# Performance work log

Measured on AMD Instinct MI355X. Metric: run time of the kernel, lower is better.

The kernel has to match this reference:

```python
import jax, jax.numpy as jnp
import numpy as np

N, D = 66560, 128      # total actor rows, embedding dim
M = 16384              # anchor count (scenes x vehicles)
P, NEG = 3, 63         # positives per anchor, negatives per anchor
EPS = 1e-8             # torch nn.CosineSimilarity eps


def setup_inputs() -> dict:
    key = jax.random.key(0)
    k1, k2, k3, k4, k5 = jax.random.split(key, 5)
    return {
        "ids_fut": jax.random.normal(k1, (N, D), dtype=jnp.float32),
        "ids_hist": jax.random.normal(k2, (N, D), dtype=jnp.float32),
        "anchor_idx": jax.random.randint(k3, (M,), 0, N),
        "pos_idx": jax.random.randint(k4, (M, P), 0, N),
        "neg_idx": jax.random.randint(k5, (M, NEG), 0, N),
    }


def _cos_plus_one(anchor, samples):
    # anchor: [M, D], samples: [M, K, D] -> cosine sim + 1, per torch CosineSimilarity
    dot = jnp.einsum("md,mkd->mk", anchor, samples)
    na = jnp.linalg.norm(anchor, axis=-1)[:, None]          # [M, 1]
    ns = jnp.linalg.norm(samples, axis=-1)                  # [M, K]
    return dot / jnp.maximum(na * ns, EPS) + 1.0


def reference(ids_fut, ids_hist, anchor_idx, pos_idx, neg_idx):
    anchor = ids_hist[anchor_idx]          # [M, D]
    pos = ids_fut[pos_idx]                 # [M, P, D]
    neg = ids_fut[neg_idx]                 # [M, NEG, D]
    sp = jnp.sum(_cos_plus_one(anchor, pos), axis=1)   # [M]
    sn = jnp.sum(_cos_plus_one(anchor, neg), axis=1)   # [M]
    sim_loss = -jnp.log(sp / (sp + sn))                 # [M]
    loss_tot = jnp.sum(sim_loss)           # 'repres_loss'; 'repres_loss_cnt' == M (constant)
    return loss_tot
```

## Files before the change

### kernel.cpp

```cpp
#include <hip/hip_runtime.h>
#include <math.h>

#define DIM 128
#define P_POS 3
#define N_NEG 63
#define SCALE 16.0f

typedef float floatx2 __attribute__((ext_vector_type(2)));

#if defined(__has_builtin)
#if __has_builtin(__builtin_elementwise_fma)
#define HAVE_EFMA 1
#endif
#endif

__device__ __forceinline__ floatx2 pkfma(floatx2 a, floatx2 b, floatx2 c) {
#ifdef HAVE_EFMA
    return __builtin_elementwise_fma(a, b, c);
#else
    floatx2 r;
    r.x = fmaf(a.x, b.x, c.x);
    r.y = fmaf(a.y, b.y, c.y);
    return r;
#endif
}

__device__ __forceinline__ float wave_reduce_sum(float v) {
#pragma unroll
    for (int off = 32; off > 0; off >>= 1) v += __shfl_xor(v, off, 64);
    return v;
}
__device__ __forceinline__ float g8_reduce(float v) {
#pragma unroll
    for (int off = 4; off > 0; off >>= 1) v += __shfl_xor(v, off, 64);
    return v;
}
__device__ __forceinline__ float g32_reduce(float v) {
#pragma unroll
    for (int off = 16; off > 0; off >>= 1) v += __shfl_xor(v, off, 64);
    return v;
}

__global__ __launch_bounds__(256) void prep_fp8_kernel(const float* __restrict__ fut,
                                                       unsigned* __restrict__ futq,
                                                       int nrows) {
    int half = threadIdx.x >> 5;
    int l = threadIdx.x & 31;
    int row = blockIdx.x * 8 + half;
    if (row >= nrows) return;
    float4 x = *reinterpret_cast<const float4*>(fut + (size_t)row * DIM + l * 4);
    float ss = x.x * x.x;
    ss = fmaf(x.y, x.y, ss);
    ss = fmaf(x.z, x.z, ss);
    ss = fmaf(x.w, x.w, ss);
    ss = g32_reduce(ss);
    float r = (ss > 0.f) ? rsqrtf(ss) * SCALE : 0.f;
    int w = __builtin_amdgcn_cvt_pk_fp8_f32(x.x * r, x.y * r, 0, false);
    w = __builtin_amdgcn_cvt_pk_fp8_f32(x.z * r, x.w * r, w, true);
    futq[(size_t)row * 32 + l] = (unsigned)w;
}

__global__ __launch_bounds__(256) void idloss_fp8w_kernel(
    const float* __restrict__ hist, const int* __restrict__ anchor_idx,
    const int* __restrict__ pos_idx, const int* __restrict__ neg_idx,
    const uint4* __restrict__ futq, float* __restrict__ partials) {
    __shared__ float smem[4];
    const int wave = threadIdx.x >> 6;
    const int lane = threadIdx.x & 63;
    const int m = __builtin_amdgcn_readfirstlane(blockIdx.x * 4 + wave);
    const int g = lane >> 3;
    const int t = lane & 7;

    int nidx = (lane < N_NEG) ? neg_idx[m * N_NEG + lane] : 0;

    const int aidx = anchor_idx[m];
    const int p0 = pos_idx[m * P_POS + 0];
    const int p1 = pos_idx[m * P_POS + 1];
    const int p2 = pos_idx[m * P_POS + 2];
    int pidx = (g == 1) ? p1 : (g == 2) ? p2 : p0;

    const float4* ap =
        reinterpret_cast<const float4*>(hist + (size_t)aidx * DIM + t * 16);
    float4 A0 = ap[0], A1 = ap[1], A2 = ap[2], A3 = ap[3];
    float ss = A0.x * A0.x;
    ss = fmaf(A0.y, A0.y, ss); ss = fmaf(A0.z, A0.z, ss); ss = fmaf(A0.w, A0.w, ss);
    ss = fmaf(A1.x, A1.x, ss); ss = fmaf(A1.y, A1.y, ss);
    ss = fmaf(A1.z, A1.z, ss); ss = fmaf(A1.w, A1.w, ss);
    ss = fmaf(A2.x, A2.x, ss); ss = fmaf(A2.y, A2.y, ss);
    ss = fmaf(A2.z, A2.z, ss); ss = fmaf(A2.w, A2.w, ss);
    ss = fmaf(A3.x, A3.x, ss); ss = fmaf(A3.y, A3.y, ss);
    ss = fmaf(A3.z, A3.z, ss); ss = fmaf(A3.w, A3.w, ss);
    ss = g8_reduce(ss);
    float rna = (ss > 0.f) ? rsqrtf(ss) * (1.0f / SCALE) : 0.f;
    floatx2 av0, av1, av2, av3, av4, av5, av6, av7;
    av0.x = A0.x * rna; av0.y = A0.y * rna;
    av1.x = A0.z * rna; av1.y = A0.w * rna;
    av2.x = A1.x * rna; av2.y = A1.y * rna;
    av3.x = A1.z * rna; av3.y = A1.w * rna;
    av4.x = A2.x * rna; av4.y = A2.y * rna;
    av5.x = A2.z * rna; av5.y = A2.w * rna;
    av6.x = A3.x * rna; av6.y = A3.y * rna;
    av7.x = A3.z * rna; av7.y = A3.w * rna;

    int js[8];
#pragma unroll
    for (int k = 0; k < 8; ++k) js[k] = __shfl(nidx, 8 * k + g, 64);

    uint4 vp = futq[(size_t)pidx * 8 + t];
    if (g >= P_POS) { vp.x = vp.y = vp.z = vp.w = 0u; }
    uint4 vs[8];
#pragma unroll
    for (int k = 0; k < 8; ++k) {
        vs[k] = futq[(size_t)js[k] * 8 + t];
        if (8 * k + g >= N_NEG) { vs[k].x = vs[k].y = vs[k].z = vs[k].w = 0u; }
    }

    floatx2 n0 = {0.f, 0.f}, n1 = {0.f, 0.f}, n2 = {0.f, 0.f}, n3 = {0.f, 0.f};
#pragma unroll
    for (int k = 0; k < 8; ++k) {
        uint4 v = vs[k];
        n0 = pkfma(__builtin_amdgcn_cvt_pk_f32_fp8(v.x, false), av0, n0);
        n1 = pkfma(__builtin_amdgcn_cvt_pk_f32_fp8(v.x, true), av1, n1);
        n2 = pkfma(__builtin_amdgcn_cvt_pk_f32_fp8(v.y, false), av2, n2);
        n3 = pkfma(__builtin_amdgcn_cvt_pk_f32_fp8(v.y, true), av3, n3);
        n0 = pkfma(__builtin_amdgcn_cvt_pk_f32_fp8(v.z, false), av4, n0);
        n1 = pkfma(__builtin_amdgcn_cvt_pk_f32_fp8(v.z, true), av5, n1);
        n2 = pkfma(__builtin_amdgcn_cvt_pk_f32_fp8(v.w, false), av6, n2);
        n3 = pkfma(__builtin_amdgcn_cvt_pk_f32_fp8(v.w, true), av7, n3);
    }
    floatx2 pa = {0.f, 0.f}, pb = {0.f, 0.f};
    pa = pkfma(__builtin_amdgcn_cvt_pk_f32_fp8(vp.x, false), av0, pa);
    pb = pkfma(__builtin_amdgcn_cvt_pk_f32_fp8(vp.x, true), av1, pb);
    pa = pkfma(__builtin_amdgcn_cvt_pk_f32_fp8(vp.y, false), av2, pa);
    pb = pkfma(__builtin_amdgcn_cvt_pk_f32_fp8(vp.y, true), av3, pb);
    pa = pkfma(__builtin_amdgcn_cvt_pk_f32_fp8(vp.z, false), av4, pa);
    pb = pkfma(__builtin_amdgcn_cvt_pk_f32_fp8(vp.z, true), av5, pb);
    pa = pkfma(__builtin_amdgcn_cvt_pk_f32_fp8(vp.w, false), av6, pa);
    pb = pkfma(__builtin_amdgcn_cvt_pk_f32_fp8(vp.w, true), av7, pb);

    floatx2 ns = (n0 + n1) + (n2 + n3);
    floatx2 ps = pa + pb;
    float accn = wave_reduce_sum(ns.x + ns.y);
    float accp = wave_reduce_sum(ps.x + ps.y);

    if (lane == 0) {
        float sp = accp + (float)P_POS;
        float sn = accn + (float)N_NEG;
        smem[wave] = -logf(sp / (sp + sn));
    }
    __syncthreads();
    if (threadIdx.x == 0)
        partials[blockIdx.x] = smem[0] + smem[1] + smem[2] + smem[3];
}

__global__ __launch_bounds__(1024) void reduce1024_kernel(
    const float* __restrict__ partials, float* __restrict__ out, int n4) {
    __shared__ float smem[16];
    const int tid = threadIdx.x;
    const int lane = tid & 63;
    const int wid = tid >> 6;
    float acc = 0.f;
    for (int i = tid; i < n4; i += 1024) {
        float4 v = reinterpret_cast<const float4*>(partials)[i];
        acc += (v.x + v.y) + (v.z + v.w);
    }
    acc = wave_reduce_sum(acc);
    if (lane == 0) smem[wid] = acc;
    __syncthreads();
    if (tid == 0) {
        float s = 0.f;
#pragma unroll
        for (int i = 0; i < 16; ++i) s += smem[i];
        out[0] = s;
    }
}

extern "C" void kernel_launch(void* const* d_in, const int* in_sizes, int n_in,
                              void* d_out, int out_size, void* d_ws, size_t ws_size,
                              hipStream_t stream) {
    const float* fut  = (const float*)d_in[0];
    const float* hist = (const float*)d_in[1];
    const int* anchor_idx = (const int*)d_in[2];
    const int* pos_idx    = (const int*)d_in[3];
    const int* neg_idx    = (const int*)d_in[4];

    int N = in_sizes[0] / DIM;
    int M = in_sizes[2];
    int main_blocks = M / 4;

    size_t futq_bytes = (size_t)N * 32 * sizeof(unsigned);
    unsigned* futq = (unsigned*)d_ws;
    float* partials = (float*)((char*)d_ws + futq_bytes);

    int prep_blocks = (N + 7) / 8;
    prep_fp8_kernel<<<prep_blocks, 256, 0, stream>>>(fut, futq, N);
    idloss_fp8w_kernel<<<main_blocks, 256, 0, stream>>>(hist, anchor_idx, pos_idx,
                                                        neg_idx, (const uint4*)futq,
                                                        partials);
    reduce1024_kernel<<<1, 1024, 0, stream>>>(partials, (float*)d_out,
                                              main_blocks / 4);
}
```

Baseline: 31.12 us.

## Process two anchors per wavefront and write per-anchor partials directly

Measured after the change: 33.42 us. 7.4% more time.

```diff
diff --git a/kernel.cpp b/kernel.cpp
--- a/kernel.cpp
+++ b/kernel.cpp
@@ -29,6 +29,15 @@
 #pragma unroll
     for (int off = 32; off > 0; off >>= 1) v += __shfl_xor(v, off, 64);
     return v;
+}
+__device__ __forceinline__ void wave_reduce4(float& a, float& b, float& c, float& d) {
+#pragma unroll
+    for (int off = 32; off > 0; off >>= 1) {
+        a += __shfl_xor(a, off, 64);
+        b += __shfl_xor(b, off, 64);
+        c += __shfl_xor(c, off, 64);
+        d += __shfl_xor(d, off, 64);
+    }
 }
 __device__ __forceinline__ float g8_reduce(float v) {
 #pragma unroll
@@ -60,97 +69,129 @@
     futq[(size_t)row * 32 + l] = (unsigned)w;
 }
 
-__global__ __launch_bounds__(256) void idloss_fp8w_kernel(
+__device__ __forceinline__ void dq8(uint4 v, const floatx2* av, floatx2& x, floatx2& y,
+                                    floatx2& z, floatx2& w) {
+    x = pkfma(__builtin_amdgcn_cvt_pk_f32_fp8(v.x, false), av[0], x);
+    y = pkfma(__builtin_amdgcn_cvt_pk_f32_fp8(v.x, true), av[1], y);
+    z = pkfma(__builtin_amdgcn_cvt_pk_f32_fp8(v.y, false), av[2], z);
+    w = pkfma(__builtin_amdgcn_cvt_pk_f32_fp8(v.y, true), av[3], w);
+    x = pkfma(__builtin_amdgcn_cvt_pk_f32_fp8(v.z, false), av[4], x);
+    y = pkfma(__builtin_amdgcn_cvt_pk_f32_fp8(v.z, true), av[5], y);
+    z = pkfma(__builtin_amdgcn_cvt_pk_f32_fp8(v.w, false), av[6], z);
+    w = pkfma(__builtin_amdgcn_cvt_pk_f32_fp8(v.w, true), av[7], w);
+}
+
+__global__ __launch_bounds__(256) void idloss_fp8d_kernel(
     const float* __restrict__ hist, const int* __restrict__ anchor_idx,
     const int* __restrict__ pos_idx, const int* __restrict__ neg_idx,
     const uint4* __restrict__ futq, float* __restrict__ partials) {
-    __shared__ float smem[4];
     const int wave = threadIdx.x >> 6;
     const int lane = threadIdx.x & 63;
-    const int m = __builtin_amdgcn_readfirstlane(blockIdx.x * 4 + wave);
+    const int m0 = __builtin_amdgcn_readfirstlane((blockIdx.x * 4 + wave) * 2);
+    const int m1 = m0 + 1;
     const int g = lane >> 3;
     const int t = lane & 7;
 
-    int nidx = (lane < N_NEG) ? neg_idx[m * N_NEG + lane] : 0;
-
-    const int aidx = anchor_idx[m];
-    const int p0 = pos_idx[m * P_POS + 0];
-    const int p1 = pos_idx[m * P_POS + 1];
-    const int p2 = pos_idx[m * P_POS + 2];
-    int pidx = (g == 1) ? p1 : (g == 2) ? p2 : p0;
-
-    const float4* ap =
-        reinterpret_cast<const float4*>(hist + (size_t)aidx * DIM + t * 16);
-    float4 A0 = ap[0], A1 = ap[1], A2 = ap[2], A3 = ap[3];
-    float ss = A0.x * A0.x;
-    ss = fmaf(A0.y, A0.y, ss); ss = fmaf(A0.z, A0.z, ss); ss = fmaf(A0.w, A0.w, ss);
-    ss = fmaf(A1.x, A1.x, ss); ss = fmaf(A1.y, A1.y, ss);
-    ss = fmaf(A1.z, A1.z, ss); ss = fmaf(A1.w, A1.w, ss);
-    ss = fmaf(A2.x, A2.x, ss); ss = fmaf(A2.y, A2.y, ss);
-    ss = fmaf(A2.z, A2.z, ss); ss = fmaf(A2.w, A2.w, ss);
-    ss = fmaf(A3.x, A3.x, ss); ss = fmaf(A3.y, A3.y, ss);
-    ss = fmaf(A3.z, A3.z, ss); ss = fmaf(A3.w, A3.w, ss);
-    ss = g8_reduce(ss);
-    float rna = (ss > 0.f) ? rsqrtf(ss) * (1.0f / SCALE) : 0.f;
-    floatx2 av0, av1, av2, av3, av4, av5, av6, av7;
-    av0.x = A0.x * rna; av0.y = A0.y * rna;
-    av1.x = A0.z * rna; av1.y = A0.w * rna;
-    av2.x = A1.x * rna; av2.y = A1.y * rna;
-    av3.x = A1.z * rna; av3.y = A1.w * rna;
-    av4.x = A2.x * rna; av4.y = A2.y * rna;
-    av5.x = A2.z * rna; av5.y = A2.w * rna;
-    av6.x = A3.x * rna; av6.y = A3.y * rna;
-    av7.x = A3.z * rna; av7.y = A3.w * rna;
-
-    int js[8];
-#pragma unroll
-    for (int k = 0; k < 8; ++k) js[k] = __shfl(nidx, 8 * k + g, 64);
-
-    uint4 vp = futq[(size_t)pidx * 8 + t];
-    if (g >= P_POS) { vp.x = vp.y = vp.z = vp.w = 0u; }
-    uint4 vs[8];
+    int nidx0 = (lane < N_NEG) ? neg_idx[m0 * N_NEG + lane] : 0;
+    int nidx1 = (lane < N_NEG) ? neg_idx[m1 * N_NEG + lane] : 0;
+    const int aidx0 = anchor_idx[m0];
+    const int aidx1 = anchor_idx[m1];
+    const int p00 = pos_idx[m0 * P_POS + 0];
+    const int p01 = pos_idx[m0 * P_POS + 1];
+    const int p02 = pos_idx[m0 * P_POS + 2];
+    const int p10 = pos_idx[m1 * P_POS + 0];
+    const int p11 = pos_idx[m1 * P_POS + 1];
+    const int p12 = pos_idx[m1 * P_POS + 2];
+    int pidx0 = (g == 1) ? p01 : (g == 2) ? p02 : p00;
+    int pidx1 = (g == 1) ? p11 : (g == 2) ? p12 : p10;
+
+    const float4* apA =
+        reinterpret_cast<const float4*>(hist + (size_t)aidx0 * DIM + t * 16);
+    const float4* apB =
+        reinterpret_cast<const float4*>(hist + (size_t)aidx1 * DIM + t * 16);
+    float4 A[4], B[4];
+#pragma unroll
+    for (int i = 0; i < 4; ++i) A[i] = apA[i];
+#pragma unroll
+    for (int i = 0; i < 4; ++i) B[i] = apB[i];
+
+    float ssA = 0.f, ssB = 0.f;
+#pragma unroll
+    for (int i = 0; i < 4; ++i) {
+        ssA = fmaf(A[i].x, A[i].x, ssA); ssA = fmaf(A[i].y, A[i].y, ssA);
+        ssA = fmaf(A[i].z, A[i].z, ssA); ssA = fmaf(A[i].w, A[i].w, ssA);
+        ssB = fmaf(B[i].x, B[i].x, ssB); ssB = fmaf(B[i].y, B[i].y, ssB);
+        ssB = fmaf(B[i].z, B[i].z, ssB); ssB = fmaf(B[i].w, B[i].w, ssB);
+    }
+    ssA = g8_reduce(ssA);
+    ssB = g8_reduce(ssB);
+    float rnaA = (ssA > 0.f) ? rsqrtf(ssA) * (1.0f / SCALE) : 0.f;
+    float rnaB = (ssB > 0.f) ? rsqrtf(ssB) * (1.0f / SCALE) : 0.f;
+    floatx2 avA[8], avB[8];
+#pragma unroll
+    for (int i = 0; i < 4; ++i) {
+        avA[2 * i].x = A[i].x * rnaA; avA[2 * i].y = A[i].y * rnaA;
+        avA[2 * i + 1].x = A[i].z * rnaA; avA[2 * i + 1].y = A[i].w * rnaA;
+        avB[2 * i].x = B[i].x * rnaB; avB[2 * i].y = B[i].y * rnaB;
+        avB[2 * i + 1].x = B[i].z * rnaB; avB[2 * i + 1].y = B[i].w * rnaB;
+    }
+
+    int jsA[8], jsB[8];
+#pragma unroll
+    for (int k = 0; k < 8; ++k) jsA[k] = __shfl(nidx0, 8 * k + g, 64);
+#pragma unroll
+    for (int k = 0; k < 8; ++k) jsB[k] = __shfl(nidx1, 8 * k + g, 64);
+
+    uint4 vpA = futq[(size_t)pidx0 * 8 + t];
+    uint4 vpB = futq[(size_t)pidx1 * 8 + t];
+    if (g >= P_POS) {
+        vpA.x = vpA.y = vpA.z = vpA.w = 0u;
+        vpB.x = vpB.y = vpB.z = vpB.w = 0u;
+    }
+    uint4 vsA[8], vsB[8];
 #pragma unroll
     for (int k = 0; k < 8; ++k) {
-        vs[k] = futq[(size_t)js[k] * 8 + t];
-        if (8 * k + g >= N_NEG) { vs[k].x = vs[k].y = vs[k].z = vs[k].w = 0u; }
-    }
-
-    floatx2 n0 = {0.f, 0.f}, n1 = {0.f, 0.f}, n2 = {0.f, 0.f}, n3 = {0.f, 0.f};
+        vsA[k] = futq[(size_t)jsA[k] * 8 + t];
+        if (8 * k + g >= N_NEG) { vsA[k].x = vsA[k].y = vsA[k].z = vsA[k].w = 0u; }
+    }
 #pragma unroll
     for (int k = 0; k < 8; ++k) {
-        uint4 v = vs[k];
-        n0 = pkfma(__builtin_amdgcn_cvt_pk_f32_fp8(v.x, false), av0, n0);
-        n1 = pkfma(__builtin_amdgcn_cvt_pk_f32_fp8(v.x, true), av1, n1);
-        n2 = pkfma(__builtin_amdgcn_cvt_pk_f32_fp8(v.y, false), av2, n2);
-        n3 = pkfma(__builtin_amdgcn_cvt_pk_f32_fp8(v.y, true), av3, n3);
-        n0 = pkfma(__builtin_amdgcn_cvt_pk_f32_fp8(v.z, false), av4, n0);
-        n1 = pkfma(__builtin_amdgcn_cvt_pk_f32_fp8(v.z, true), av5, n1);
-        n2 = pkfma(__builtin_amdgcn_cvt_pk_f32_fp8(v.w, false), av6, n2);
-        n3 = pkfma(__builtin_amdgcn_cvt_pk_f32_fp8(v.w, true), av7, n3);
-    }
-    floatx2 pa = {0.f, 0.f}, pb = {0.f, 0.f};
-    pa = pkfma(__builtin_amdgcn_cvt_pk_f32_fp8(vp.x, false), av0, pa);
-    pb = pkfma(__builtin_amdgcn_cvt_pk_f32_fp8(vp.x, true), av1, pb);
-    pa = pkfma(__builtin_amdgcn_cvt_pk_f32_fp8(vp.y, false), av2, pa);
-    pb = pkfma(__builtin_amdgcn_cvt_pk_f32_fp8(vp.y, true), av3, pb);
-    pa = pkfma(__builtin_amdgcn_cvt_pk_f32_fp8(vp.z, false), av4, pa);
-    pb = pkfma(__builtin_amdgcn_cvt_pk_f32_fp8(vp.z, true), av5, pb);
-    pa = pkfma(__builtin_amdgcn_cvt_pk_f32_fp8(vp.w, false), av6, pa);
-    pb = pkfma(__builtin_amdgcn_cvt_pk_f32_fp8(vp.w, true), av7, pb);
-
-    floatx2 ns = (n0 + n1) + (n2 + n3);
-    floatx2 ps = pa + pb;
-    float accn = wave_reduce_sum(ns.x + ns.y);
-    float accp = wave_reduce_sum(ps.x + ps.y);
+        vsB[k] = futq[(size_t)jsB[k] * 8 + t];
+        if (8 * k + g >= N_NEG) { vsB[k].x = vsB[k].y = vsB[k].z = vsB[k].w = 0u; }
+    }
+
+    floatx2 nA0 = {0.f, 0.f}, nA1 = {0.f, 0.f}, nA2 = {0.f, 0.f}, nA3 = {0.f, 0.f};
+#pragma unroll
+    for (int k = 0; k < 8; ++k) dq8(vsA[k], avA, nA0, nA1, nA2, nA3);
+    floatx2 pA0 = {0.f, 0.f}, pA1 = {0.f, 0.f}, pA2 = {0.f, 0.f}, pA3 = {0.f, 0.f};
+    dq8(vpA, avA, pA0, pA1, pA2, pA3);
+
+    floatx2 nB0 = {0.f, 0.f}, nB1 = {0.f, 0.f}, nB2 = {0.f, 0.f}, nB3 = {0.f, 0.f};
+#pragma unroll
+    for (int k = 0; k < 8; ++k) dq8(vsB[k], avB, nB0, nB1, nB2, nB3);
+    floatx2 pB0 = {0.f, 0.f}, pB1 = {0.f, 0.f}, pB2 = {0.f, 0.f}, pB3 = {0.f, 0.f};
+    dq8(vpB, avB, pB0, pB1, pB2, pB3);
+
+    floatx2 nsA = (nA0 + nA1) + (nA2 + nA3);
+    floatx2 psA = (pA0 + pA1) + (pA2 + pA3);
+    floatx2 nsB = (nB0 + nB1) + (nB2 + nB3);
+    floatx2 psB = (pB0 + pB1) + (pB2 + pB3);
+    float accnA = nsA.x + nsA.y;
+    float accpA = psA.x + psA.y;
+    float accnB = nsB.x + nsB.y;
+    float accpB = psB.x + psB.y;
+    wave_reduce4(accnA, accpA, accnB, accpB);
 
     if (lane == 0) {
-        float sp = accp + (float)P_POS;
-        float sn = accn + (float)N_NEG;
-        smem[wave] = -logf(sp / (sp + sn));
-    }
-    __syncthreads();
-    if (threadIdx.x == 0)
-        partials[blockIdx.x] = smem[0] + smem[1] + smem[2] + smem[3];
+        float spA = accpA + (float)P_POS;
+        float snA = accnA + (float)N_NEG;
+        float spB = accpB + (float)P_POS;
+        float snB = accnB + (float)N_NEG;
+        float2 r;
+        r.x = -logf(spA / (spA + snA));
+        r.y = -logf(spB / (spB + snB));
+        *reinterpret_cast<float2*>(partials + m0) = r;
+    }
 }
 
 __global__ __launch_bounds__(1024) void reduce1024_kernel(
@@ -186,7 +227,7 @@
 
     int N = in_sizes[0] / DIM;
     int M = in_sizes[2];
-    int main_blocks = M / 4;
+    int main_blocks = M / 8;
 
     size_t futq_bytes = (size_t)N * 32 * sizeof(unsigned);
     unsigned* futq = (unsigned*)d_ws;
@@ -194,9 +235,8 @@
 
     int prep_blocks = (N + 7) / 8;
     prep_fp8_kernel<<<prep_blocks, 256, 0, stream>>>(fut, futq, N);
-    idloss_fp8w_kernel<<<main_blocks, 256, 0, stream>>>(hist, anchor_idx, pos_idx,
+    idloss_fp8d_kernel<<<main_blocks, 256, 0, stream>>>(hist, anchor_idx, pos_idx,
                                                         neg_idx, (const uint4*)futq,
                                                         partials);
-    reduce1024_kernel<<<1, 1024, 0, stream>>>(partials, (float*)d_out,
-                                              main_blocks / 4);
-}
+    reduce1024_kernel<<<1, 1024, 0, stream>>>(partials, (float*)d_out, M / 4);
+}
```
